# Kernel optimization log

Measured on AMD Instinct MI355X. Metric: run time of the kernel, lower is better.

The kernel has to match this reference:

```python
import jax, jax.numpy as jnp
import numpy as np

H = W = 56
WS = 7            # window size
SHIFT = 3
HEADS = 6
DIM = 192
N = WS * WS       # tokens per window (49)
NW = (H // WS) * (W // WS)  # windows per image (64)
EPS = 1e-5


def _rel_pos_index():
    coords = np.stack(np.meshgrid(np.arange(WS), np.arange(WS), indexing='ij'))
    cf = coords.reshape(2, -1)
    rel = (cf[:, :, None] - cf[:, None, :]).transpose(1, 2, 0)
    rel[:, :, 0] += WS - 1
    rel[:, :, 1] += WS - 1
    rel[:, :, 0] *= 2 * WS - 1
    return rel.sum(-1).astype(np.int32)  # [N, N]


def _attn_mask():
    img = np.zeros([1, H, W, 1], dtype=np.float32)
    slices = (slice(0, -WS), slice(-WS, -SHIFT), slice(-SHIFT, None))
    cnt = 0
    for hs in slices:
        for ws_ in slices:
            img[:, hs, ws_, :] = cnt
            cnt += 1
    m = img.reshape(1, H // WS, WS, W // WS, WS, 1).transpose(0, 1, 3, 2, 4, 5)
    m = m.reshape(-1, N)                      # [nW, N]
    diff = m[:, None, :] - m[:, :, None]
    return np.where(diff != 0, -100.0, 0.0).astype(np.float32)  # [nW, N, N]

_RPI = _rel_pos_index()
_MASK = _attn_mask()


def _ln(x, g, b):
    mu = jnp.mean(x, axis=-1, keepdims=True)
    var = jnp.mean(jnp.square(x - mu), axis=-1, keepdims=True)
    return (x - mu) * jax.lax.rsqrt(var + EPS) * g + b


def setup_inputs() -> dict:
    key = jax.random.key(0)
    ks = jax.random.split(key, 12)
    C, Hd = DIM, DIM * 4
    s = lambda n: 1.0 / np.sqrt(n)
    return {
        'x': jax.random.normal(ks[0], (32, H * W, C), jnp.float32),
        'norm1_g': jnp.ones((C,), jnp.float32),
        'norm1_b': jnp.zeros((C,), jnp.float32),
        'qkv_w': jax.random.normal(ks[1], (C, 3 * C), jnp.float32) * s(C),
        'qkv_b': jnp.zeros((3 * C,), jnp.float32),
        'bias_table': jax.random.normal(ks[2], ((2 * WS - 1) ** 2, HEADS), jnp.float32) * 0.02,
        'proj_w': jax.random.normal(ks[3], (C, C), jnp.float32) * s(C),
        'proj_b': jnp.zeros((C,), jnp.float32),
        'norm2_g': jnp.ones((C,), jnp.float32),
        'norm2_b': jnp.zeros((C,), jnp.float32),
        'fc1_w': jax.random.normal(ks[4], (C, Hd), jnp.float32) * s(C),
        'fc1_b': jnp.zeros((Hd,), jnp.float32),
        'fc2_w': jax.random.normal(ks[5], (Hd, C), jnp.float32) * s(Hd),
        'fc2_b': jnp.zeros((C,), jnp.float32),
    }


def reference(x, norm1_g, norm1_b, qkv_w, qkv_b, bias_table, proj_w, proj_b,
              norm2_g, norm2_b, fc1_w, fc1_b, fc2_w, fc2_b):
    B, L, C = x.shape
    hd = C // HEADS
    scale = hd ** -0.5

    shortcut = x
    h = _ln(x, norm1_g, norm1_b).reshape(B, H, W, C)
    h = jnp.roll(h, (-SHIFT, -SHIFT), axis=(1, 2))

    # window partition -> [B*nW, N, C]
    h = h.reshape(B, H // WS, WS, W // WS, WS, C).transpose(0, 1, 3, 2, 4, 5)
    xw = h.reshape(B * NW, N, C)

    qkv = (xw @ qkv_w + qkv_b).reshape(B * NW, N, 3, HEADS, hd)
    q, k, v = jnp.moveaxis(qkv, 2, 0)                 # each [B*nW, N, H, d]
    q = jnp.swapaxes(q, 1, 2) * scale                 # [B*nW, H, N, d]
    k = jnp.swapaxes(k, 1, 2)
    v = jnp.swapaxes(v, 1, 2)

    attn = jnp.einsum('whnd,whmd->whnm', q, k)        # [B*nW, H, N, N]
    bias = bias_table[jnp.asarray(_RPI).reshape(-1)].reshape(N, N, HEADS)
    attn = attn + jnp.transpose(bias, (2, 0, 1))[None]
    mask = jnp.asarray(_MASK)                         # [nW, N, N]
    attn = attn.reshape(B, NW, HEADS, N, N) + mask[None, :, None]
    attn = jax.nn.softmax(attn.reshape(B * NW, HEADS, N, N), axis=-1)

    out = jnp.einsum('whnm,whmd->whnd', attn, v)      # [B*nW, H, N, d]
    out = jnp.swapaxes(out, 1, 2).reshape(B * NW, N, C)
    out = out @ proj_w + proj_b

    # window reverse -> [B, H, W, C]
    out = out.reshape(B, H // WS, W // WS, WS, WS, C).transpose(0, 1, 3, 2, 4, 5)
    out = out.reshape(B, H, W, C)
    out = jnp.roll(out, (SHIFT, SHIFT), axis=(1, 2)).reshape(B, L, C)

    x = shortcut + out
    hmlp = _ln(x, norm2_g, norm2_b)
    hmlp = jax.nn.gelu(hmlp @ fc1_w + fc1_b, approximate=False) @ fc2_w + fc2_b
    return x + hmlp
```

## Files before the change

### kernel.cpp

```cpp
#include <hip/hip_runtime.h>
#include <hip/hip_bf16.h>
#include <math.h>

static constexpr int CB     = 32;
static constexpr int CH     = 56;
static constexpr int CW     = 56;
static constexpr int CC     = 192;
static constexpr int CSHIFT = 3;
static constexpr int CN     = 49;
static constexpr int CNW    = 64;
static constexpr int CL     = CH * CW;
static constexpr int CM     = CB * CNW * CN;
static constexpr int CHID   = 768;

typedef __attribute__((ext_vector_type(8))) __bf16 bf16x8;
typedef __attribute__((ext_vector_type(4))) float  f32x4;

__device__ __forceinline__ float bfu2f(unsigned short u) {
  union { unsigned i; float f; } c; c.i = (unsigned)u << 16; return c.f;
}
__device__ __forceinline__ unsigned short f2bu(float f) {
  __hip_bfloat16 b = __float2bfloat16(f);
  return *(unsigned short*)&b;
}
__device__ __forceinline__ float gelu_fast(float v) {
  float s  = v * v;
  float u2 = v * fmaf(s, 0.0713548163f, 1.5957691216f);
  float e  = __expf(u2);
  float t  = 1.0f - __fdividef(2.0f, e + 1.0f);
  float h  = 0.5f * v;
  return fmaf(h, t, h);
}

#define GLOAD16(g, l) __builtin_amdgcn_global_load_lds( \
    (__attribute__((address_space(1))) void*)(g),       \
    (__attribute__((address_space(3))) void*)(l), 16, 0, 0)

__global__ __launch_bounds__(256)
void prep_kernel(const float* __restrict__ qkv_w, const float* __restrict__ proj_w,
                 const float* __restrict__ fc1_w, const float* __restrict__ fc2_w,
                 const float* __restrict__ btab,
                 __hip_bfloat16* __restrict__ wq, __hip_bfloat16* __restrict__ wp,
                 __hip_bfloat16* __restrict__ w1, __hip_bfloat16* __restrict__ w2,
                 float* __restrict__ bias2)
{
  int idx = blockIdx.x * 256 + threadIdx.x;
  if (idx < 110592) {
    int k = idx / 576, n = idx - k * 576;
    wq[n * 192 + k] = __float2bfloat16(qkv_w[idx]);
    return;
  }
  idx -= 110592;
  if (idx < 36864) {
    int k = idx / 192, n = idx - k * 192;
    wp[n * 192 + k] = __float2bfloat16(proj_w[idx]);
    return;
  }
  idx -= 36864;
  if (idx < 147456) {
    int k = idx / 768, n = idx - k * 768;
    w1[n * 192 + k] = __float2bfloat16(fc1_w[idx]);
    return;
  }
  idx -= 147456;
  if (idx < 147456) {
    int k = idx / 192, n = idx - k * 192;
    w2[n * 768 + k] = __float2bfloat16(fc2_w[idx]);
    return;
  }
  idx -= 147456;
  if (idx < 98304) {
    int j = idx & 63, i = (idx >> 6) & 63;
    int rest = idx >> 12;
    int h = rest % 6, wt = rest / 6;
    float val;
    if (i >= 49 || j >= 49) {
      val = -INFINITY;
    } else {
      int ti = i / 7, ci = i - ti * 7;
      int tj = j / 7, cj = j - tj * 7;
      val = btab[((ti - tj + 6) * 13 + (ci - cj + 6)) * 6 + h];
      int hri = (wt & 2) ? ((ti < 4) ? 1 : 2) : 0;
      int hci = (wt & 1) ? ((ci < 4) ? 1 : 2) : 0;
      int hrj = (wt & 2) ? ((tj < 4) ? 1 : 2) : 0;
      int hcj = (wt & 1) ? ((cj < 4) ? 1 : 2) : 0;
      if (hri * 3 + hci != hrj * 3 + hcj) val -= 100.0f;
    }
    bias2[idx] = val;
  }
}

template<bool ROLL>
__global__ __launch_bounds__(256)
void ln_kernel(const float* __restrict__ xin, const float* __restrict__ gamma,
               const float* __restrict__ beta, __hip_bfloat16* __restrict__ out)
{
  const int wid = threadIdx.x >> 6, lane = threadIdx.x & 63;
  const int m = blockIdx.x * 4 + wid;
  size_t src;
  if (ROLL) {
    int b   = m / (CNW * CN);
    int rem = m - b * (CNW * CN);
    int nw  = rem / CN, t = rem - nw * CN;
    int wr = nw >> 3, wc = nw & 7;
    int ti = t / 7, tj = t - ti * 7;
    int sr = wr * 7 + ti + CSHIFT; if (sr >= CH) sr -= CH;
    int sc = wc * 7 + tj + CSHIFT; if (sc >= CW) sc -= CW;
    src = ((size_t)b * CL + (size_t)sr * CW + sc) * CC;
  } else {
    src = (size_t)m * CC;
  }
  float v0 = xin[src + lane], v1 = xin[src + lane + 64], v2 = xin[src + lane + 128];
  float s  = v0 + v1 + v2;
  float sq = v0 * v0 + v1 * v1 + v2 * v2;
  #pragma unroll
  for (int off = 32; off; off >>= 1) { s += __shfl_xor(s, off); sq += __shfl_xor(sq, off); }
  const float mu  = s * (1.0f / CC);
  const float inv = rsqrtf(sq * (1.0f / CC) - mu * mu + 1e-5f);
  const size_t dst = (size_t)m * CC;
  out[dst + lane      ] = __float2bfloat16((v0 - mu) * inv * gamma[lane      ] + beta[lane      ]);
  out[dst + lane + 64 ] = __float2bfloat16((v1 - mu) * inv * gamma[lane + 64 ] + beta[lane + 64 ]);
  out[dst + lane + 128] = __float2bfloat16((v2 - mu) * inv * gamma[lane + 128] + beta[lane + 128]);
}

template<int MODE>
__global__ __launch_bounds__(256)
void gemm_mfma(const __hip_bfloat16* __restrict__ Ain, const __hip_bfloat16* __restrict__ Wt,
               const float* __restrict__ bias, void* __restrict__ Outv,
               const float* __restrict__ resid, int K, int Ncols)
{
  __shared__ short As[128 * 64];
  __shared__ short Bs[64 * 64];

  const int tid  = threadIdx.x;
  const int lane = tid & 63, wid = tid >> 6;

  const int nbx = gridDim.x;
  const int nwg = nbx * gridDim.y;
  const int wg  = blockIdx.y * nbx + blockIdx.x;
  const int swz = (wg & 7) * (nwg >> 3) + (wg >> 3);
  const int row0 = (swz / nbx) * 128, col0 = (swz % nbx) * 64;

  const int wm = wid >> 1, wn = wid & 1;
  const int lr = lane & 15, lg = lane >> 4;

  const short* A  = (const short*)Ain;
  const short* W  = (const short*)Wt;

  f32x4 acc[4][2] = {};

  for (int kk = 0; kk < K; kk += 64) {
    #pragma unroll
    for (int it = 0; it < 4; ++it) {
      int c = it * 256 + tid;
      int row = c >> 3, slot = c & 7;
      int kg = (slot ^ (row & 7)) * 8;
      GLOAD16(A + (size_t)(row0 + row) * K + kk + kg, As + c * 8);
    }
    #pragma unroll
    for (int it = 0; it < 2; ++it) {
      int c = it * 256 + tid;
      int row = c >> 3, slot = c & 7;
      int kg = (slot ^ (row & 7)) * 8;
      GLOAD16(W + (size_t)(col0 + row) * K + kk + kg, Bs + c * 8);
    }
    __syncthreads();

    #pragma unroll
    for (int kh = 0; kh < 2; ++kh) {
      const int sb = kh * 4 + lg;
      bf16x8 bfr[2];
      #pragma unroll
      for (int n = 0; n < 2; ++n) {
        int br = wn * 32 + n * 16 + lr;
        int slot = sb ^ (br & 7);
        bfr[n] = *(const bf16x8*)(Bs + br * 64 + slot * 8);
      }
      #pragma unroll
      for (int m = 0; m < 4; ++m) {
        int ar = wm * 64 + m * 16 + lr;
        int slot = sb ^ (ar & 7);
        bf16x8 afr = *(const bf16x8*)(As + ar * 64 + slot * 8);
        acc[m][0] = __builtin_amdgcn_mfma_f32_16x16x32_bf16(afr, bfr[0], acc[m][0], 0, 0, 0);
        acc[m][1] = __builtin_amdgcn_mfma_f32_16x16x32_bf16(afr, bfr[1], acc[m][1], 0, 0, 0);
      }
    }
    __syncthreads();
  }

  const int colA = col0 + wn * 32 + lr;
  const float bv0 = bias[colA];
  const float bv1 = bias[colA + 16];
  #pragma unroll
  for (int m = 0; m < 4; ++m) {
    #pragma unroll
    for (int r = 0; r < 4; ++r) {
      const int mrow = row0 + wm * 64 + m * 16 + lg * 4 + r;
      const float v0 = acc[m][0][r] + bv0;
      const float v1 = acc[m][1][r] + bv1;
      if (MODE == 0) {
        __hip_bfloat16* O = (__hip_bfloat16*)Outv;
        const size_t rr = (size_t)mrow * Ncols;
        O[rr + colA]      = __float2bfloat16(v0);
        O[rr + colA + 16] = __float2bfloat16(v1);
      } else if (MODE == 1) {
        int b = mrow / (CNW * CN);
        int rem = mrow - b * (CNW * CN);
        int nw = rem / CN, t = rem - nw * CN;
        int wr = nw >> 3, wc = nw & 7;
        int ti = t / 7, tj = t - ti * 7;
        int dr = wr * 7 + ti + CSHIFT; if (dr >= CH) dr -= CH;
        int dc = wc * 7 + tj + CSHIFT; if (dc >= CW) dc -= CW;
        const size_t dst = ((size_t)b * CL + (size_t)dr * CW + dc) * CC;
        float* O = (float*)Outv;
        O[dst + colA]      = resid[dst + colA]      + v0;
        O[dst + colA + 16] = resid[dst + colA + 16] + v1;
      } else if (MODE == 2) {
        __hip_bfloat16* O = (__hip_bfloat16*)Outv;
        const size_t rr = (size_t)mrow * Ncols;
        O[rr + colA]      = __float2bfloat16(gelu_fast(v0));
        O[rr + colA + 16] = __float2bfloat16(gelu_fast(v1));
      } else {
        float* O = (float*)Outv;
        const size_t rr = (size_t)mrow * Ncols;
        O[rr + colA]      = resid[rr + colA]      + v0;
        O[rr + colA + 16] = resid[rr + colA + 16] + v1;
      }
    }
  }
}

__global__ __launch_bounds__(64)
void attn_mfma_kernel(const __hip_bfloat16* __restrict__ qkv,
                      const float* __restrict__ bias2,
                      __hip_bfloat16* __restrict__ attnout)
{
  __shared__ unsigned short VT[32 * 72];
  __shared__ unsigned short Pl[64 * 72];

  const int bid = blockIdx.x;
  const int w = bid / 6, h = bid - (bid / 6) * 6;
  const int lane = threadIdx.x;
  const int lr = lane & 15, lg = lane >> 4;
  const int nw = w & 63;
  const int wt = (((nw >> 3) == 7) ? 2 : 0) + (((nw & 7) == 7) ? 1 : 0);
  const unsigned short* Q = (const unsigned short*)qkv;
  const size_t rowbase = (size_t)w * 49 * 576;
  const float scale = 0.17677669529663687f;

  for (int e = lane; e < 196; e += 64) {
    int t = e % 49, c = e / 49;
    uint4 v = *(const uint4*)(Q + rowbase + (size_t)t * 576 + 384 + h * 32 + c * 8);
    unsigned va[4] = {v.x, v.y, v.z, v.w};
    #pragma unroll
    for (int q = 0; q < 4; ++q) {
      VT[(c * 8 + q * 2    ) * 72 + t] = (unsigned short)(va[q] & 0xffff);
      VT[(c * 8 + q * 2 + 1) * 72 + t] = (unsigned short)(va[q] >> 16);
    }
  }
  for (int e = lane; e < 32 * 15; e += 64) {
    int d = e / 15, t = 49 + e - (e / 15) * 15;
    VT[d * 72 + t] = 0;
  }

  bf16x8 qf[4], kf[4];
  #pragma unroll
  for (int it = 0; it < 4; ++it) {
    int tok = it * 16 + lr; if (tok > 48) tok = 48;
    qf[it] = *(const bf16x8*)(Q + rowbase + (size_t)tok * 576 + h * 32 + lg * 8);
  }
  #pragma unroll
  for (int jt = 0; jt < 4; ++jt) {
    int tok = jt * 16 + lr; if (tok > 48) tok = 48;
    kf[jt] = *(const bf16x8*)(Q + rowbase + (size_t)tok * 576 + 192 + h * 32 + lg * 8);
  }

  f32x4 acc[4][4] = {};
  #pragma unroll
  for (int jt = 0; jt < 4; ++jt)
    #pragma unroll
    for (int it = 0; it < 4; ++it)
      acc[jt][it] = __builtin_amdgcn_mfma_f32_16x16x32_bf16(kf[jt], qf[it], acc[jt][it], 0, 0, 0);

  __syncthreads();

  const float* brow = bias2 + ((size_t)(wt * 6 + h) * 64) * 64;
  #pragma unroll
  for (int it = 0; it < 4; ++it) {
    const int i = it * 16 + lr;
    float s[4][4];
    #pragma unroll
    for (int jt = 0; jt < 4; ++jt) {
      float4 bv = *(const float4*)(brow + (size_t)i * 64 + jt * 16 + lg * 4);
      s[jt][0] = fmaf(acc[jt][it][0], scale, bv.x);
      s[jt][1] = fmaf(acc[jt][it][1], scale, bv.y);
      s[jt][2] = fmaf(acc[jt][it][2], scale, bv.z);
      s[jt][3] = fmaf(acc[jt][it][3], scale, bv.w);
    }
    float mx = s[0][0];
    #pragma unroll
    for (int jt = 0; jt < 4; ++jt)
      #pragma unroll
      for (int r = 0; r < 4; ++r) mx = fmaxf(mx, s[jt][r]);
    mx = fmaxf(mx, __shfl_xor(mx, 16));
    mx = fmaxf(mx, __shfl_xor(mx, 32));
    float sum = 0.0f;
    #pragma unroll
    for (int jt = 0; jt < 4; ++jt)
      #pragma unroll
      for (int r = 0; r < 4; ++r) { s[jt][r] = __expf(s[jt][r] - mx); sum += s[jt][r]; }
    sum += __shfl_xor(sum, 16);
    sum += __shfl_xor(sum, 32);
    const float inv = 1.0f / sum;
    #pragma unroll
    for (int jt = 0; jt < 4; ++jt) {
      unsigned lo = (unsigned)f2bu(s[jt][0] * inv) | ((unsigned)f2bu(s[jt][1] * inv) << 16);
      unsigned hi = (unsigned)f2bu(s[jt][2] * inv) | ((unsigned)f2bu(s[jt][3] * inv) << 16);
      uint2 val; val.x = lo; val.y = hi;
      *(uint2*)&Pl[i * 72 + jt * 16 + lg * 4] = val;
    }
  }

  __syncthreads();

  f32x4 o[4][2] = {};
  #pragma unroll
  for (int ks = 0; ks < 2; ++ks) {
    bf16x8 pa[4], vb[2];
    #pragma unroll
    for (int it = 0; it < 4; ++it)
      pa[it] = *(const bf16x8*)&Pl[(it * 16 + lr) * 72 + ks * 32 + lg * 8];
    #pragma unroll
    for (int nt = 0; nt < 2; ++nt)
      vb[nt] = *(const bf16x8*)&VT[(nt * 16 + lr) * 72 + ks * 32 + lg * 8];
    #pragma unroll
    for (int it = 0; it < 4; ++it) {
      o[it][0] = __builtin_amdgcn_mfma_f32_16x16x32_bf16(pa[it], vb[0], o[it][0], 0, 0, 0);
      o[it][1] = __builtin_amdgcn_mfma_f32_16x16x32_bf16(pa[it], vb[1], o[it][1], 0, 0, 0);
    }
  }

  #pragma unroll
  for (int it = 0; it < 4; ++it) {
    #pragma unroll
    for (int r = 0; r < 4; ++r) {
      int i = it * 16 + lg * 4 + r;
      if (i < 49) {
        size_t dst = ((size_t)w * 49 + i) * 192 + h * 32;
        attnout[dst + lr]      = __float2bfloat16(o[it][0][r]);
        attnout[dst + 16 + lr] = __float2bfloat16(o[it][1][r]);
      }
    }
  }
}

extern "C" void kernel_launch(void* const* d_in, const int* in_sizes, int n_in,
                              void* d_out, int out_size, void* d_ws, size_t ws_size,
                              hipStream_t stream)
{
  const float* x        = (const float*)d_in[0];
  const float* n1g      = (const float*)d_in[1];
  const float* n1b      = (const float*)d_in[2];
  const float* qkv_w    = (const float*)d_in[3];
  const float* qkv_b    = (const float*)d_in[4];
  const float* btab     = (const float*)d_in[5];
  const float* proj_w   = (const float*)d_in[6];
  const float* proj_b   = (const float*)d_in[7];
  const float* n2g      = (const float*)d_in[8];
  const float* n2b      = (const float*)d_in[9];
  const float* fc1_w    = (const float*)d_in[10];
  const float* fc1_b    = (const float*)d_in[11];
  const float* fc2_w    = (const float*)d_in[12];
  const float* fc2_b    = (const float*)d_in[13];
  float* out = (float*)d_out;

  char* ws = (char*)d_ws;
  const size_t szA = (size_t)CM * CC * 2;
  const size_t szB = (size_t)CM * CHID * 2;
  __hip_bfloat16* bufA = (__hip_bfloat16*)ws;
  __hip_bfloat16* bufB = (__hip_bfloat16*)(ws + szA);
  __hip_bfloat16* wq   = (__hip_bfloat16*)(ws + szA + szB);
  __hip_bfloat16* wp   = wq + 576 * 192;
  __hip_bfloat16* w1   = wp + 192 * 192;
  __hip_bfloat16* w2   = w1 + 768 * 192;
  float* bias2         = (float*)(w2 + 192 * 768);

  prep_kernel<<<(110592 + 36864 + 147456 + 147456 + 98304 + 255) / 256, 256, 0, stream>>>(
      qkv_w, proj_w, fc1_w, fc2_w, btab, wq, wp, w1, w2, bias2);

  ln_kernel<true><<<CM / 4, 256, 0, stream>>>(x, n1g, n1b, bufA);
  gemm_mfma<0><<<dim3(576 / 64, CM / 128), 256, 0, stream>>>(bufA, wq, qkv_b, bufB, nullptr, CC, 576);
  attn_mfma_kernel<<<2048 * 6, 64, 0, stream>>>(bufB, bias2, bufA);
  gemm_mfma<1><<<dim3(192 / 64, CM / 128), 256, 0, stream>>>(bufA, wp, proj_b, out, x, CC, 192);
  ln_kernel<false><<<CM / 4, 256, 0, stream>>>(out, n2g, n2b, bufA);
  gemm_mfma<2><<<dim3(CHID / 64, CM / 128), 256, 0, stream>>>(bufA, w1, fc1_b, bufB, nullptr, CC, CHID);
  gemm_mfma<3><<<dim3(192 / 64, CM / 128), 256, 0, stream>>>(bufB, w2, fc2_b, out, out, CHID, 192);
}
```

Baseline: 349.5 us.

## Fuse fc1-GELU-fc2 MLP into one kernel and enlarge GEMM row tiles

Adds a fused MLP kernel. Each block keeps a 64-row slice of the normalized activations in registers, computes fc1 plus GELU in 192-wide hidden chunks staged through shared memory, and accumulates fc2 directly. This avoids writing and re-reading the 768-wide hidden tensor to global memory and drops one launch. The generic GEMM moves from 128x64 to 256x64 tiles, each wave owning 64 rows by 64 columns. The fused kernel has no double buffering and heavy register use (24 f32x4 accumulators), which may limit occupancy, and the bigger GEMM tiles halve the grid size.

```diff
diff --git a/kernel.cpp b/kernel.cpp
--- a/kernel.cpp
+++ b/kernel.cpp
@@ -129,7 +129,7 @@
                const float* __restrict__ bias, void* __restrict__ Outv,
                const float* __restrict__ resid, int K, int Ncols)
 {
-  __shared__ short As[128 * 64];
+  __shared__ short As[256 * 64];
   __shared__ short Bs[64 * 64];
 
   const int tid  = threadIdx.x;
@@ -139,19 +139,18 @@
   const int nwg = nbx * gridDim.y;
   const int wg  = blockIdx.y * nbx + blockIdx.x;
   const int swz = (wg & 7) * (nwg >> 3) + (wg >> 3);
-  const int row0 = (swz / nbx) * 128, col0 = (swz % nbx) * 64;
-
-  const int wm = wid >> 1, wn = wid & 1;
+  const int row0 = (swz / nbx) * 256, col0 = (swz % nbx) * 64;
+
   const int lr = lane & 15, lg = lane >> 4;
 
   const short* A  = (const short*)Ain;
   const short* W  = (const short*)Wt;
 
-  f32x4 acc[4][2] = {};
+  f32x4 acc[4][4] = {};
 
   for (int kk = 0; kk < K; kk += 64) {
     #pragma unroll
-    for (int it = 0; it < 4; ++it) {
+    for (int it = 0; it < 8; ++it) {
       int c = it * 256 + tid;
       int row = c >> 3, slot = c & 7;
       int kg = (slot ^ (row & 7)) * 8;
@@ -169,41 +168,40 @@
     #pragma unroll
     for (int kh = 0; kh < 2; ++kh) {
       const int sb = kh * 4 + lg;
-      bf16x8 bfr[2];
-      #pragma unroll
-      for (int n = 0; n < 2; ++n) {
-        int br = wn * 32 + n * 16 + lr;
-        int slot = sb ^ (br & 7);
-        bfr[n] = *(const bf16x8*)(Bs + br * 64 + slot * 8);
+      bf16x8 bfr[4];
+      #pragma unroll
+      for (int nt = 0; nt < 4; ++nt) {
+        int br = nt * 16 + lr;
+        bfr[nt] = *(const bf16x8*)(Bs + br * 64 + (sb ^ (br & 7)) * 8);
       }
       #pragma unroll
       for (int m = 0; m < 4; ++m) {
-        int ar = wm * 64 + m * 16 + lr;
-        int slot = sb ^ (ar & 7);
-        bf16x8 afr = *(const bf16x8*)(As + ar * 64 + slot * 8);
-        acc[m][0] = __builtin_amdgcn_mfma_f32_16x16x32_bf16(afr, bfr[0], acc[m][0], 0, 0, 0);
-        acc[m][1] = __builtin_amdgcn_mfma_f32_16x16x32_bf16(afr, bfr[1], acc[m][1], 0, 0, 0);
+        int ar = wid * 64 + m * 16 + lr;
+        bf16x8 afr = *(const bf16x8*)(As + ar * 64 + (sb ^ (ar & 7)) * 8);
+        #pragma unroll
+        for (int nt = 0; nt < 4; ++nt)
+          acc[m][nt] = __builtin_amdgcn_mfma_f32_16x16x32_bf16(afr, bfr[nt], acc[m][nt], 0, 0, 0);
       }
     }
     __syncthreads();
   }
 
-  const int colA = col0 + wn * 32 + lr;
-  const float bv0 = bias[colA];
-  const float bv1 = bias[colA + 16];
+  float bv[4];
+  #pragma unroll
+  for (int nt = 0; nt < 4; ++nt) bv[nt] = bias[col0 + nt * 16 + lr];
+
   #pragma unroll
   for (int m = 0; m < 4; ++m) {
     #pragma unroll
     for (int r = 0; r < 4; ++r) {
-      const int mrow = row0 + wm * 64 + m * 16 + lg * 4 + r;
-      const float v0 = acc[m][0][r] + bv0;
-      const float v1 = acc[m][1][r] + bv1;
+      const int mrow = row0 + wid * 64 + m * 16 + lg * 4 + r;
       if (MODE == 0) {
         __hip_bfloat16* O = (__hip_bfloat16*)Outv;
-        const size_t rr = (size_t)mrow * Ncols;
-        O[rr + colA]      = __float2bfloat16(v0);
-        O[rr + colA + 16] = __float2bfloat16(v1);
-      } else if (MODE == 1) {
+        const size_t rr = (size_t)mrow * Ncols + col0 + lr;
+        #pragma unroll
+        for (int nt = 0; nt < 4; ++nt)
+          O[rr + nt * 16] = __float2bfloat16(acc[m][nt][r] + bv[nt]);
+      } else {
         int b = mrow / (CNW * CN);
         int rem = mrow - b * (CNW * CN);
         int nw = rem / CN, t = rem - nw * CN;
@@ -211,21 +209,108 @@
         int ti = t / 7, tj = t - ti * 7;
         int dr = wr * 7 + ti + CSHIFT; if (dr >= CH) dr -= CH;
         int dc = wc * 7 + tj + CSHIFT; if (dc >= CW) dc -= CW;
-        const size_t dst = ((size_t)b * CL + (size_t)dr * CW + dc) * CC;
+        const size_t dst = ((size_t)b * CL + (size_t)dr * CW + dc) * CC + col0 + lr;
         float* O = (float*)Outv;
-        O[dst + colA]      = resid[dst + colA]      + v0;
-        O[dst + colA + 16] = resid[dst + colA + 16] + v1;
-      } else if (MODE == 2) {
-        __hip_bfloat16* O = (__hip_bfloat16*)Outv;
-        const size_t rr = (size_t)mrow * Ncols;
-        O[rr + colA]      = __float2bfloat16(gelu_fast(v0));
-        O[rr + colA + 16] = __float2bfloat16(gelu_fast(v1));
-      } else {
-        float* O = (float*)Outv;
-        const size_t rr = (size_t)mrow * Ncols;
-        O[rr + colA]      = resid[rr + colA]      + v0;
-        O[rr + colA + 16] = resid[rr + colA + 16] + v1;
-      }
+        #pragma unroll
+        for (int nt = 0; nt < 4; ++nt)
+          O[dst + nt * 16] = resid[dst + nt * 16] + acc[m][nt][r] + bv[nt];
+      }
+    }
+  }
+}
+
+__global__ __launch_bounds__(256)
+void mlp_kernel(const __hip_bfloat16* __restrict__ h2, const __hip_bfloat16* __restrict__ w1,
+                const float* __restrict__ b1, const __hip_bfloat16* __restrict__ w2,
+                const float* __restrict__ b2, float* __restrict__ out)
+{
+  __shared__ short Bs[192 * 64];
+  __shared__ short Hch[64 * 200];
+
+  const int tid = threadIdx.x, lane = tid & 63, wv = tid >> 6;
+  const int lr = lane & 15, lg = lane >> 4;
+  const int m0 = blockIdx.x * 64;
+  const short* A  = (const short*)h2;
+  const short* W1 = (const short*)w1;
+  const short* W2 = (const short*)w2;
+
+  const short* arow = A + (size_t)(m0 + wv * 16 + lr) * 192 + lg * 8;
+  bf16x8 af[6];
+  #pragma unroll
+  for (int j = 0; j < 6; ++j) af[j] = *(const bf16x8*)(arow + j * 32);
+
+  f32x4 acc2[12] = {};
+
+  for (int ch = 0; ch < 4; ++ch) {
+    f32x4 acc[12] = {};
+    #pragma unroll
+    for (int ksl = 0; ksl < 3; ++ksl) {
+      #pragma unroll
+      for (int it = 0; it < 6; ++it) {
+        int c = it * 256 + tid;
+        int col = c >> 3, slot = c & 7;
+        int kg = (slot ^ (col & 7)) * 8;
+        GLOAD16(W1 + (size_t)(ch * 192 + col) * 192 + ksl * 64 + kg, Bs + c * 8);
+      }
+      __syncthreads();
+      #pragma unroll
+      for (int kh = 0; kh < 2; ++kh) {
+        const int sb = kh * 4 + lg;
+        const bf16x8 a = af[ksl * 2 + kh];
+        #pragma unroll
+        for (int cf = 0; cf < 12; ++cf) {
+          int bc = cf * 16 + lr;
+          bf16x8 b = *(const bf16x8*)(Bs + bc * 64 + (sb ^ (bc & 7)) * 8);
+          acc[cf] = __builtin_amdgcn_mfma_f32_16x16x32_bf16(a, b, acc[cf], 0, 0, 0);
+        }
+      }
+      __syncthreads();
+    }
+    #pragma unroll
+    for (int cf = 0; cf < 12; ++cf) {
+      int col = cf * 16 + lr;
+      float bv = b1[ch * 192 + col];
+      #pragma unroll
+      for (int r = 0; r < 4; ++r) {
+        int row = wv * 16 + lg * 4 + r;
+        Hch[row * 200 + col] = (short)f2bu(gelu_fast(acc[cf][r] + bv));
+      }
+    }
+    __syncthreads();
+    #pragma unroll
+    for (int ksl = 0; ksl < 3; ++ksl) {
+      #pragma unroll
+      for (int it = 0; it < 6; ++it) {
+        int c = it * 256 + tid;
+        int col = c >> 3, slot = c & 7;
+        int kg = (slot ^ (col & 7)) * 8;
+        GLOAD16(W2 + (size_t)col * 768 + ch * 192 + ksl * 64 + kg, Bs + c * 8);
+      }
+      __syncthreads();
+      #pragma unroll
+      for (int kh = 0; kh < 2; ++kh) {
+        const int sb = kh * 4 + lg;
+        bf16x8 a = *(const bf16x8*)(Hch + (wv * 16 + lr) * 200 + ksl * 64 + kh * 32 + lg * 8);
+        #pragma unroll
+        for (int cf = 0; cf < 12; ++cf) {
+          int bc = cf * 16 + lr;
+          bf16x8 b = *(const bf16x8*)(Bs + bc * 64 + (sb ^ (bc & 7)) * 8);
+          acc2[cf] = __builtin_amdgcn_mfma_f32_16x16x32_bf16(a, b, acc2[cf], 0, 0, 0);
+        }
+      }
+      __syncthreads();
+    }
+  }
+
+  #pragma unroll
+  for (int cf = 0; cf < 12; ++cf) {
+    int col = cf * 16 + lr;
+    float bv = b2[col];
+    #pragma unroll
+    for (int r = 0; r < 4; ++r) {
+      int row = wv * 16 + lg * 4 + r;
+      size_t idx = (size_t)(m0 + row) * 192 + col;
+      out[idx] += acc2[cf][r] + bv;
     }
   }
 }
@@ -376,7 +461,7 @@
 
   char* ws = (char*)d_ws;
   const size_t szA = (size_t)CM * CC * 2;
-  const size_t szB = (size_t)CM * CHID * 2;
+  const size_t szB = (size_t)CM * 576 * 2;
   __hip_bfloat16* bufA = (__hip_bfloat16*)ws;
   __hip_bfloat16* bufB = (__hip_bfloat16*)(ws + szA);
   __hip_bfloat16* wq   = (__hip_bfloat16*)(ws + szA + szB);
@@ -389,10 +474,9 @@
       qkv_w, proj_w, fc1_w, fc2_w, btab, wq, wp, w1, w2, bias2);
 
   ln_kernel<true><<<CM / 4, 256, 0, stream>>>(x, n1g, n1b, bufA);
-  gemm_mfma<0><<<dim3(576 / 64, CM / 128), 256, 0, stream>>>(bufA, wq, qkv_b, bufB, nullptr, CC, 576);
+  gemm_mfma<0><<<dim3(576 / 64, CM / 256), 256, 0, stream>>>(bufA, wq, qkv_b, bufB, nullptr, CC, 576);
   attn_mfma_kernel<<<2048 * 6, 64, 0, stream>>>(bufB, bias2, bufA);
-  gemm_mfma<1><<<dim3(192 / 64, CM / 128), 256, 0, stream>>>(bufA, wp, proj_b, out, x, CC, 192);
+  gemm_mfma<1><<<dim3(192 / 64, CM / 256), 256, 0, stream>>>(bufA, wp, proj_b, out, x, CC, 192);
   ln_kernel<false><<<CM / 4, 256, 0, stream>>>(out, n2g, n2b, bufA);
-  gemm_mfma<2><<<dim3(CHID / 64, CM / 128), 256, 0, stream>>>(bufA, w1, fc1_b, bufB, nullptr, CC, CHID);
-  gemm_mfma<3><<<dim3(192 / 64, CM / 128), 256, 0, stream>>>(bufB, w2, fc2_b, out, out, CHID, 192);
-}
+  mlp_kernel<<<CM / 64, 256, 0, stream>>>(bufA, w1, fc1_b, w2, fc2_b, out);
+}
```

New measurement: 409.1 us. 17.1% more time.
